# Optimization experiments

Measured on AMD Instinct MI355X. Metric: run time of the kernel, lower is better.

## Reference

```python
import jax, jax.numpy as jnp
import numpy as np

MIN_NORM = 1e-15
BALL_EPS = 4e-3  # float32 boundary eps used by the PoincareBall manifold


def _norm(x):
    return jnp.maximum(jnp.linalg.norm(x, axis=-1, keepdims=True), MIN_NORM)


def _artanh(x):
    # clamp like torch Artanh autograd fn (1e-7 margin)
    return jnp.arctanh(jnp.clip(x, -1.0 + 1e-7, 1.0 - 1e-7))


def proj(x, c):
    n = _norm(x)
    maxnorm = (1.0 - BALL_EPS) / jnp.sqrt(c)
    return jnp.where(n > maxnorm, x / n * maxnorm, x)


def expmap0(u, c):
    sc = jnp.sqrt(c)
    n = _norm(u)
    return jnp.tanh(sc * n) * u / (sc * n)


def logmap0(p, c):
    sc = jnp.sqrt(c)
    n = _norm(p)
    return _artanh(sc * n) * p / (sc * n)


def mobius_add(x, y, c):
    x2 = jnp.sum(x * x, axis=-1, keepdims=True)
    y2 = jnp.sum(y * y, axis=-1, keepdims=True)
    xy = jnp.sum(x * y, axis=-1, keepdims=True)
    num = (1.0 + 2.0 * c * xy + c * y2) * x + (1.0 - c * x2) * y
    denom = 1.0 + 2.0 * c * xy + c * c * x2 * y2
    return num / jnp.maximum(denom, MIN_NORM)


def mobius_matvec(m, x, c):
    sc = jnp.sqrt(c)
    xn = _norm(x)
    mx = x @ m.T  # [N, out]
    mxn = _norm(mx)
    res = jnp.tanh(mxn / xn * _artanh(sc * xn)) * mx / (mxn * sc)
    is_zero = jnp.all(mx == 0, axis=-1, keepdims=True)
    return jnp.where(is_zero, jnp.zeros_like(res), res)


def setup_inputs() -> dict:
    key = jax.random.key(0)
    N, D_IN, D_OUT, E = 100000, 128, 128, 1600000
    k1, k2, k3, k4, k5 = jax.random.split(key, 5)
    # points inside the Poincare ball (||x|| ~ 0.34 < 1)
    x = 0.03 * jax.random.normal(k1, (N, D_IN), dtype=jnp.float32)
    # xavier_uniform with gain sqrt(2)
    limit = np.sqrt(2.0) * np.sqrt(6.0 / (D_IN + D_OUT))
    weight = jax.random.uniform(k2, (D_OUT, D_IN), minval=-limit, maxval=limit, dtype=jnp.float32)
    bias = jnp.zeros((D_OUT,), dtype=jnp.float32)
    edge_index = jax.random.randint(k3, (2, E), 0, N, dtype=jnp.int64)
    edge_weight = jax.random.uniform(k4, (E,), dtype=jnp.float32) / 16.0
    return {"x": x, "weight": weight, "bias": bias,
            "edge_index": edge_index, "edge_weight": edge_weight,
            "num_nodes": N}


def reference(x, weight, bias, edge_index, edge_weight, num_nodes):
    c_in = 1.0
    c_out = 1.0
    # --- OriginHypLinear (dropout=0 / eval) ---
    mv = proj(mobius_matvec(weight, x, c_in), c_in)
    hyp_bias = proj(expmap0(bias[None, :], c_in), c_in)  # proj_tan0 is identity
    h = proj(mobius_add(mv, hyp_bias, c_in), c_in)
    # --- OriginHypAgg: logmap0 -> spmm -> expmap0 ---
    xt = logmap0(h, c_in)
    dst, src = edge_index[0], edge_index[1]
    support = jax.ops.segment_sum(edge_weight[:, None] * xt[src], dst,
                                  num_segments=num_nodes)
    h = proj(expmap0(support, c_in), c_in)
    # --- OriginHypAct: relu in tangent space ---
    xt = jax.nn.relu(logmap0(h, c_in))  # proj_tan0 identity
    return proj(expmap0(xt, c_out), c_out)
```

## Files before the change

### kernel.cpp

```cpp
#include <hip/hip_runtime.h>
#include <math.h>

#define D 128
#define MAXNORM 0.996f
#define MINNORM 1e-15f
#define ATCLAMP (1.0f - 1e-7f)

#define CHUNK 2048
#define BSH   7
#define MAXNB 1024

typedef unsigned int   u32;
typedef unsigned short u16;

typedef __attribute__((ext_vector_type(8))) short bf16x8;
typedef __attribute__((ext_vector_type(4))) float f32x4;

__device__ __forceinline__ float wsum(float v) {
#pragma unroll
  for (int m = 32; m; m >>= 1) v += __shfl_xor(v, m);
  return v;
}
__device__ __forceinline__ float rsum16(float v) {
#pragma unroll
  for (int m = 1; m <= 8; m <<= 1) v += __shfl_xor(v, m);
  return v;
}

__device__ __forceinline__ float frcp(float x) { return __builtin_amdgcn_rcpf(x); }

__device__ __forceinline__ float fast_artanh(float x) {
  x = fminf(x, ATCLAMP);
  return 0.5f * __logf((1.0f + x) * frcp(1.0f - x));
}
__device__ __forceinline__ float fast_tanh(float z) {
  float t = __expf(-2.0f * z);
  return (1.0f - t) * frcp(1.0f + t);
}

__device__ __forceinline__ float bflo(u32 u) { return __uint_as_float(u << 16); }
__device__ __forceinline__ float bfhi(u32 u) { return __uint_as_float(u & 0xffff0000u); }
__device__ __forceinline__ u16 f2bf(float f) {
  u32 u = __float_as_uint(f);
  return (u16)((u + 0x7fffu + ((u >> 16) & 1u)) >> 16);
}
__device__ __forceinline__ float bf2f(u16 h) { return __uint_as_float(((u32)h) << 16); }

union U4B8 { uint4 u; bf16x8 b; };
__device__ __forceinline__ bf16x8 as_b8(uint4 v) { U4B8 c; c.u = v; return c.b; }

__device__ __forceinline__ bool detect_bf16(const u32* p) {
  float lo = fabsf(bflo(p[threadIdx.x & 63]));
  return (bool)__all(lo < 1.0f);
}
__device__ __forceinline__ bool detect_i64(const int* p) {
  return (bool)__all(p[2 * (threadIdx.x & 63) + 1] == 0);
}

template<bool BF>
__device__ __forceinline__ void k1_body(const void* xv, const void* Wv,
                                        const void* bv, u16* xt, int N,
                                        uint4* Wh, uint4* Wl) {
  const int tid  = threadIdx.x;
  const int lane = tid & 63;
  const int wid  = tid >> 6;
  const int qg   = lane >> 4;
  const int lc   = lane & 15;

  for (int slot = tid; slot < 2048; slot += 256) {
    const int l = slot & 63, frag = slot >> 6;
    const int t = frag >> 2, ks = frag & 3;
    const int j  = (l & 15) + 16 * t;
    const int k0 = 32 * ks + 8 * (l >> 4);
    if (BF) {
      Wh[slot] = ((const uint4*)Wv)[j * 16 + (k0 >> 3)];
    } else {
      const float* Wf = (const float*)Wv;
      float4 f0 = *(const float4*)(Wf + (size_t)j * D + k0);
      float4 f1 = *(const float4*)(Wf + (size_t)j * D + k0 + 4);
      float f[8] = {f0.x, f0.y, f0.z, f0.w, f1.x, f1.y, f1.z, f1.w};
      u32 hw[4], lw[4];
#pragma unroll
      for (int i = 0; i < 4; ++i) {
        u16 h0 = f2bf(f[2*i]),  h1 = f2bf(f[2*i+1]);
        u16 l0 = f2bf(f[2*i]   - bf2f(h0));
        u16 l1 = f2bf(f[2*i+1] - bf2f(h1));
        hw[i] = (u32)h0 | ((u32)h1 << 16);
        lw[i] = (u32)l0 | ((u32)l1 << 16);
      }
      Wh[slot] = make_uint4(hw[0], hw[1], hw[2], hw[3]);
      Wl[slot] = make_uint4(lw[0], lw[1], lw[2], lw[3]);
    }
  }

  float bfr[8];
  float nb2 = 0.f;
#pragma unroll
  for (int t = 0; t < 8; ++t) {
    float v = BF ? bf2f(((const u16*)bv)[lc + 16 * t])
                 : ((const float*)bv)[lc + 16 * t];
    bfr[t] = v; nb2 += v * v;
  }
  nb2 = rsum16(nb2);
  float y2;
  {
    float nb = fmaxf(sqrtf(nb2), MINNORM);
    float s  = fast_tanh(nb) * frcp(nb);
    float n1 = s * nb;
    if (n1 > MAXNORM) s *= MAXNORM * frcp(n1);
#pragma unroll
    for (int t = 0; t < 8; ++t) bfr[t] *= s;
    y2 = s * s * nb2;
  }
  const bool bias_zero = (y2 == 0.0f);

  __syncthreads();

  const int tile  = blockIdx.x * 4 + wid;
  const int rbase = tile * 16;
  if (rbase >= N) return;

  int rowA = rbase + lc; if (rowA >= N) rowA = N - 1;
  uint4 Ah[4], Al[4];
  float xn2 = 0.f;
  if (BF) {
    const uint4* xr = (const uint4*)((const u16*)xv + (size_t)rowA * D);
#pragma unroll
    for (int ks = 0; ks < 4; ++ks) {
      uint4 v = xr[4 * ks + qg];
      Ah[ks] = v;
      float a0 = bflo(v.x), a1 = bfhi(v.x), a2 = bflo(v.y), a3 = bfhi(v.y);
      float a4 = bflo(v.z), a5 = bfhi(v.z), a6 = bflo(v.w), a7 = bfhi(v.w);
      xn2 += a0*a0 + a1*a1 + a2*a2 + a3*a3 + a4*a4 + a5*a5 + a6*a6 + a7*a7;
    }
  } else {
    const float4* xr = (const float4*)((const float*)xv + (size_t)rowA * D);
#pragma unroll
    for (int ks = 0; ks < 4; ++ks) {
      float4 f0 = xr[8 * ks + 2 * qg], f1 = xr[8 * ks + 2 * qg + 1];
      float f[8] = {f0.x, f0.y, f0.z, f0.w, f1.x, f1.y, f1.z, f1.w};
      u32 hw[4], lw[4];
#pragma unroll
      for (int i = 0; i < 4; ++i) {
        u16 h0 = f2bf(f[2*i]),  h1 = f2bf(f[2*i+1]);
        u16 l0 = f2bf(f[2*i]   - bf2f(h0));
        u16 l1 = f2bf(f[2*i+1] - bf2f(h1));
        hw[i] = (u32)h0 | ((u32)h1 << 16);
        lw[i] = (u32)l0 | ((u32)l1 << 16);
        xn2 += f[2*i] * f[2*i] + f[2*i+1] * f[2*i+1];
      }
      Ah[ks] = make_uint4(hw[0], hw[1], hw[2], hw[3]);
      Al[ks] = make_uint4(lw[0], lw[1], lw[2], lw[3]);
    }
  }
  xn2 += __shfl_xor(xn2, 16);
  xn2 += __shfl_xor(xn2, 32);

  f32x4 acc[8];
  const f32x4 zero = {0.f, 0.f, 0.f, 0.f};
#pragma unroll
  for (int t = 0; t < 8; ++t) acc[t] = zero;
#pragma unroll
  for (int ks = 0; ks < 4; ++ks) {
    bf16x8 a = as_b8(Ah[ks]);
    bf16x8 al;
    if (!BF) al = as_b8(Al[ks]);
#pragma unroll
    for (int t = 0; t < 8; ++t) {
      const int idx = (t * 4 + ks) * 64 + lane;
      bf16x8 bh = as_b8(Wh[idx]);
      acc[t] = __builtin_amdgcn_mfma_f32_16x16x32_bf16(a, bh, acc[t], 0, 0, 0);
      if (!BF) {
        bf16x8 bl = as_b8(Wl[idx]);
        acc[t] = __builtin_amdgcn_mfma_f32_16x16x32_bf16(al, bh, acc[t], 0, 0, 0);
        acc[t] = __builtin_amdgcn_mfma_f32_16x16x32_bf16(a,  bl, acc[t], 0, 0, 0);
      }
    }
  }

#pragma unroll
  for (int q = 0; q < 4; ++q) {
    const int row_off = qg * 4 + q;
    const int row = rbase + row_off;
    float xnq = fmaxf(sqrtf(__shfl(xn2, row_off)), MINNORM);
    float s2 = 0.f;
#pragma unroll
    for (int t = 0; t < 8; ++t) { float v = acc[t][q]; s2 += v * v; }
    s2 = rsum16(s2);
    float mxn = fmaxf(sqrtf(s2), MINNORM);
    float r = fast_tanh(mxn * frcp(xnq) * fast_artanh(xnq)) * frcp(mxn);
    float pn = r * mxn;
    if (pn > MAXNORM) { r *= MAXNORM * frcp(pn); pn = MAXNORM; }
    float h[8];
    float hn;
    if (bias_zero) {
#pragma unroll
      for (int t = 0; t < 8; ++t) h[t] = r * acc[t][q];
      hn = pn;
    } else {
      float xy = 0.f;
#pragma unroll
      for (int t = 0; t < 8; ++t) { h[t] = r * acc[t][q]; xy += h[t] * bfr[t]; }
      xy = rsum16(xy);
      float x2 = pn * pn;
      float ca = 1.f + 2.f * xy + y2;
      float cb = 1.f - x2;
      float id = frcp(fmaxf(1.f + 2.f * xy + x2 * y2, MINNORM));
      float s3 = 0.f;
#pragma unroll
      for (int t = 0; t < 8; ++t) { h[t] = (ca * h[t] + cb * bfr[t]) * id; s3 += h[t] * h[t]; }
      hn = fmaxf(sqrtf(rsum16(s3)), MINNORM);
    }
    float ps = (hn > MAXNORM) ? (MAXNORM * frcp(hn)) : 1.f;
    float np = fmaxf(hn * ps, MINNORM);
    float tsc = fast_artanh(np) * frcp(np) * ps;
    if (row < N) {
      u16* xo = xt + (size_t)row * D + lc;
#pragma unroll
      for (int t = 0; t < 8; ++t) xo[16 * t] = f2bf(tsc * h[t]);
    }
  }
}

extern "C" __global__ __launch_bounds__(256)
void OriginHyperbolicGraphConvolution_38628935860614_kernel(
    const void* x, const void* W, const void* b, u16* xt, int N) {
  __shared__ uint4 Wh[2048];
  __shared__ uint4 Wl[2048];
  if (detect_bf16((const u32*)x)) k1_body<true >(x, W, b, xt, N, Wh, Wl);
  else                            k1_body<false>(x, W, b, xt, N, Wh, Wl);
}

extern "C" __global__ __launch_bounds__(256) void ks1a(
    const int* ei, u16* cnt, int E, int N, int nb) {
  __shared__ int hist[MAXNB];
  const bool i64 = detect_i64(ei);
  const int tid = threadIdx.x;
  const int cbase = blockIdx.x * CHUNK;
  for (int i = tid; i < MAXNB; i += 256) hist[i] = 0;
  __syncthreads();
#pragma unroll
  for (int r = 0; r < 8; ++r) {
    const int e = cbase + r * 256 + tid;
    if (e < E) {
      int dst, src;
      if (i64) { dst = ei[2 * (size_t)e]; src = ei[2 * ((size_t)E + e)]; }
      else     { dst = ei[e];             src = ei[(size_t)E + e]; }
      if ((unsigned)dst < (unsigned)N && (unsigned)src < (unsigned)N)
        atomicAdd(&hist[dst >> BSH], 1);
    }
  }
  __syncthreads();
  u16* row = cnt + (size_t)blockIdx.x * nb;
  for (int b = tid; b < nb; b += 256) row[b] = (u16)hist[b];
}

extern "C" __global__ __launch_bounds__(256) void ks2sum(
    const u16* cnt, int* btot, int nb, int nchunks) {
  __shared__ int red[256];
  const int b = blockIdx.x, tid = threadIdx.x;
  int s = 0;
  for (int c = tid; c < nchunks; c += 256) s += cnt[(size_t)c * nb + b];
  red[tid] = s; __syncthreads();
#pragma unroll
  for (int off = 128; off; off >>= 1) {
    if (tid < off) red[tid] += red[tid + off];
    __syncthreads();
  }
  if (tid == 0) btot[b] = red[0];
}

extern "C" __global__ __launch_bounds__(1024) void ks2scan(
    const int* btot, int* bbase, int* cursor, int nb) {
  __shared__ int sc[1024];
  const int t = threadIdx.x;
  int v = (t < nb) ? btot[t] : 0;
  sc[t] = v; __syncthreads();
#pragma unroll
  for (int off = 1; off < 1024; off <<= 1) {
    int u = (t >= off) ? sc[t - off] : 0;
    __syncthreads();
    sc[t] += u;
    __syncthreads();
  }
  if (t < nb) { int o = sc[t] - v; bbase[t] = o; cursor[t] = o; }
  if (t == 1023) bbase[nb] = sc[1023];
}

extern "C" __global__ __launch_bounds__(256) void ks1b(
    const int* ei, const void* ew, int* cursor, uint2* ebuck, int E, int N, int nb) {
  __shared__ int   hist[MAXNB];
  __shared__ int   sArr[MAXNB + 1];
  __shared__ int   psum[256];
  __shared__ uint2 recs[CHUNK];
  __shared__ u16   bof[CHUNK];
  const bool i64 = detect_i64(ei);
  const bool bf  = detect_bf16((const u32*)ew);
  const int tid   = threadIdx.x;
  const int cbase = blockIdx.x * CHUNK;

  for (int i = tid; i < MAXNB; i += 256) hist[i] = 0;
  __syncthreads();

  int bkt[8], rank[8]; u32 px[8], wb[8]; bool val[8];
#pragma unroll
  for (int r = 0; r < 8; ++r) {
    const int e = cbase + r * 256 + tid;
    val[r] = false;
    if (e < E) {
      int dst, src;
      if (i64) { dst = ei[2 * (size_t)e]; src = ei[2 * ((size_t)E + e)]; }
      else     { dst = ei[e];             src = ei[(size_t)E + e]; }
      if ((unsigned)dst < (unsigned)N && (unsigned)src < (unsigned)N) {
        val[r] = true;
        bkt[r] = dst >> BSH;
        px[r]  = (u32)src | ((u32)(dst & ((1 << BSH) - 1)) << 17);
        float w;
        if (bf) w = bf2f(((const u16*)ew)[e]); else w = ((const float*)ew)[e];
        wb[r] = __float_as_uint(w);
        rank[r] = atomicAdd(&hist[bkt[r]], 1);
      }
    }
  }
  __syncthreads();

  const int g0 = tid * 4;
  int loc[4], ts = 0;
#pragma unroll
  for (int i = 0; i < 4; ++i) { loc[i] = ts; ts += hist[g0 + i]; }
  psum[tid] = ts; __syncthreads();
#pragma unroll
  for (int off = 1; off < 256; off <<= 1) {
    int t = (tid >= off) ? psum[tid - off] : 0;
    __syncthreads();
    psum[tid] += t;
    __syncthreads();
  }
  const int excl = psum[tid] - ts;
#pragma unroll
  for (int i = 0; i < 4; ++i) sArr[g0 + i] = excl + loc[i];
  if (tid == 255) sArr[MAXNB] = psum[255];
  __syncthreads();

#pragma unroll
  for (int r = 0; r < 8; ++r) if (val[r]) {
    const int idx = sArr[bkt[r]] + rank[r];
    recs[idx] = make_uint2(px[r], wb[r]);
    bof[idx]  = (u16)bkt[r];
  }
  __syncthreads();

  for (int b = tid; b < nb; b += 256) {
    const int c = sArr[b + 1] - sArr[b];
    if (c > 0) hist[b] = atomicAdd(&cursor[b], c);
  }
  const int vcnt = sArr[nb];
  __syncthreads();

  for (int i = tid; i < vcnt; i += 256) {
    const int b = bof[i];
    ebuck[hist[b] + (i - sArr[b])] = recs[i];
  }
}

extern "C" __global__ __launch_bounds__(256) void ks3(
    const uint2* ebuck, const int* bbase, uint2* esrt, int* offs, int N, int nb) {
  __shared__ int hist[128];
  __shared__ int sc[128];
  __shared__ int cur[128];
  const int tid = threadIdx.x;
  const int b = blockIdx.x;
  const int s0 = bbase[b], s1 = bbase[b + 1];
  const int node0 = b << BSH;
  if (tid < 128) hist[tid] = 0;
  __syncthreads();
  for (int i = s0 + tid; i < s1; i += 256)
    atomicAdd(&hist[(ebuck[i].x >> 17) & 127], 1);
  __syncthreads();
  int v = 0;
  if (tid < 128) { v = hist[tid]; sc[tid] = v; }
  __syncthreads();
#pragma unroll
  for (int off = 1; off < 128; off <<= 1) {
    int t = (tid < 128 && tid >= off) ? sc[tid - off] : 0;
    __syncthreads();
    if (tid < 128) sc[tid] += t;
    __syncthreads();
  }
  if (tid < 128) {
    const int st = sc[tid] - v;
    cur[tid] = st;
    const int node = node0 + tid;
    if (node < N) offs[node] = s0 + st;
  }
  if (tid == 0 && b == nb - 1) offs[N] = s1;
  __syncthreads();
  for (int i = s0 + tid; i < s1; i += 256) {
    const uint2 r = ebuck[i];
    const int d = atomicAdd(&cur[(r.x >> 17) & 127], 1);
    esrt[s0 + d] = make_uint2(r.x & 0x1FFFFu, r.y);
  }
}

extern "C" __global__ __launch_bounds__(256) void kagg(
    const int* offs, const uint2* esrt, const u16* xt,
    void* out, const void* xdet, int N) {
  const bool bf = detect_bf16((const u32*)xdet);
  const int lane = threadIdx.x & 63;
  const int node = blockIdx.x * 4 + (threadIdx.x >> 6);
  if (node >= N) return;
  const int s0 = offs[node], s1 = offs[node + 1];
  const u32* xtw = (const u32*)xt;
  float a0 = 0.f, a1 = 0.f;
  for (int base = s0; base < s1; base += 64) {
    const int m = min(64, s1 - base);
    uint2 ed = make_uint2(0u, 0u);
    if (lane < m) ed = esrt[base + lane];
    int i = 0;
    for (; i + 4 <= m; i += 4) {
      const u32 sA = __shfl(ed.x, i),     sB = __shfl(ed.x, i + 1);
      const u32 sC = __shfl(ed.x, i + 2), sD = __shfl(ed.x, i + 3);
      const u32 uA = xtw[(size_t)sA * 64 + lane];
      const u32 uB = xtw[(size_t)sB * 64 + lane];
      const u32 uC = xtw[(size_t)sC * 64 + lane];
      const u32 uD = xtw[(size_t)sD * 64 + lane];
      const float wA = __uint_as_float(__shfl(ed.y, i));
      const float wB = __uint_as_float(__shfl(ed.y, i + 1));
      const float wC = __uint_as_float(__shfl(ed.y, i + 2));
      const float wD = __uint_as_float(__shfl(ed.y, i + 3));
      a0 += wA * bflo(uA) + wB * bflo(uB) + wC * bflo(uC) + wD * bflo(uD);
      a1 += wA * bfhi(uA) + wB * bfhi(uB) + wC * bfhi(uC) + wD * bfhi(uD);
    }
    for (; i < m; ++i) {
      const u32 s = __shfl(ed.x, i);
      const float w = __uint_as_float(__shfl(ed.y, i));
      const u32 u = xtw[(size_t)s * 64 + lane];
      a0 += w * bflo(u);
      a1 += w * bfhi(u);
    }
  }
  float n = fmaxf(sqrtf(wsum(a0 * a0 + a1 * a1)), MINNORM);
  float tn = fast_tanh(n);
  float m = tn * frcp(n);
  if (tn > MAXNORM) { m *= MAXNORM * frcp(tn); tn = MAXNORM; }
  float nn = fmaxf(tn, MINNORM);
  m *= fast_artanh(nn) * frcp(nn);
  float tA = fmaxf(m * a0, 0.f), tB = fmaxf(m * a1, 0.f);
  float nr = fmaxf(sqrtf(wsum(tA * tA + tB * tB)), MINNORM);
  float t2 = fast_tanh(nr);
  float m2 = t2 * frcp(nr);
  if (t2 > MAXNORM) m2 *= MAXNORM * frcp(t2);
  float oA = m2 * tA, oB = m2 * tB;
  if (bf) {
    u32 o = ((u32)f2bf(oA)) | (((u32)f2bf(oB)) << 16);
    ((u32*)out)[(size_t)node * 64 + lane] = o;
  } else {
    ((float2*)out)[(size_t)node * 64 + lane] = make_float2(oA, oB);
  }
}

extern "C" void kernel_launch(void* const* d_in, const int* in_sizes, int n_in,
                              void* d_out, int out_size, void* d_ws, size_t ws_size,
                              hipStream_t stream) {
  const void* x    = d_in[0];
  const void* W    = d_in[1];
  const void* bias = d_in[2];
  const int*  ei   = (const int*)d_in[3];
  const void* ew   = d_in[4];
  const int N = in_sizes[0] / D;
  const int E = in_sizes[4];
  const int nchunks = (E + CHUNK - 1) / CHUNK;
  const int nb      = (N + (1 << BSH) - 1) >> BSH;

  char* ws = (char*)d_ws;
  size_t off = 0;
  auto carve = [&](size_t bytes) { char* p = ws + off; off = (off + bytes + 255) & ~(size_t)255; return p; };
  u16*   xt     = (u16*)  carve((size_t)N * D * sizeof(u16));
  uint2* ebuck  = (uint2*)carve((size_t)E * sizeof(uint2));
  uint2* esrt   = (uint2*)carve((size_t)E * sizeof(uint2));
  u16*   cnt    = (u16*)  carve((size_t)nchunks * nb * sizeof(u16));
  int*   btot   = (int*)  carve((size_t)nb * sizeof(int));
  int*   bbase  = (int*)  carve((size_t)(nb + 1) * sizeof(int));
  int*   cursor = (int*)  carve((size_t)nb * sizeof(int));
  int*   offs   = (int*)  carve((size_t)(N + 1) * sizeof(int));

  OriginHyperbolicGraphConvolution_38628935860614_kernel<<<(N + 63) / 64, 256, 0, stream>>>(
      x, W, bias, xt, N);
  ks1a  <<<nchunks, 256, 0, stream>>>(ei, cnt, E, N, nb);
  ks2sum<<<nb, 256, 0, stream>>>(cnt, btot, nb, nchunks);
  ks2scan<<<1, 1024, 0, stream>>>(btot, bbase, cursor, nb);
  ks1b  <<<nchunks, 256, 0, stream>>>(ei, ew, cursor, ebuck, E, N, nb);
  ks3   <<<nb, 256, 0, stream>>>(ebuck, bbase, esrt, offs, N, nb);
  kagg  <<<(N + 3) / 4, 256, 0, stream>>>(offs, esrt, xt, d_out, x, N);
}
```

Baseline: 280.5 us.

## Replace two-pass bucket sort with chunk-local sort and per-bucket gather

Removes the separate histogram pass (ks1a) that read the edge index a second time. Each chunk now sorts its edges locally by bucket and writes them contiguously along with per-chunk bucket offsets. ks3 gathers each bucket's slices from every chunk into shared memory, with a fallback when a bucket exceeds the staging capacity. kagg now loads edge records directly with wave-uniform offsets and an 8-way unrolled gather instead of shuffles. The cost is many small scattered reads per bucket in ks3, and a 48KB shared staging buffer that lowers occupancy.

```diff
diff --git a/kernel.cpp b/kernel.cpp
--- a/kernel.cpp
+++ b/kernel.cpp
@@ -9,6 +9,7 @@
 #define CHUNK 2048
 #define BSH   7
 #define MAXNB 1024
+#define SCAP  6144
 
 typedef unsigned int   u32;
 typedef unsigned short u16;
@@ -231,69 +232,12 @@
   else                            k1_body<false>(x, W, b, xt, N, Wh, Wl);
 }
 
-extern "C" __global__ __launch_bounds__(256) void ks1a(
-    const int* ei, u16* cnt, int E, int N, int nb) {
-  __shared__ int hist[MAXNB];
-  const bool i64 = detect_i64(ei);
-  const int tid = threadIdx.x;
-  const int cbase = blockIdx.x * CHUNK;
-  for (int i = tid; i < MAXNB; i += 256) hist[i] = 0;
-  __syncthreads();
-#pragma unroll
-  for (int r = 0; r < 8; ++r) {
-    const int e = cbase + r * 256 + tid;
-    if (e < E) {
-      int dst, src;
-      if (i64) { dst = ei[2 * (size_t)e]; src = ei[2 * ((size_t)E + e)]; }
-      else     { dst = ei[e];             src = ei[(size_t)E + e]; }
-      if ((unsigned)dst < (unsigned)N && (unsigned)src < (unsigned)N)
-        atomicAdd(&hist[dst >> BSH], 1);
-    }
-  }
-  __syncthreads();
-  u16* row = cnt + (size_t)blockIdx.x * nb;
-  for (int b = tid; b < nb; b += 256) row[b] = (u16)hist[b];
-}
-
-extern "C" __global__ __launch_bounds__(256) void ks2sum(
-    const u16* cnt, int* btot, int nb, int nchunks) {
-  __shared__ int red[256];
-  const int b = blockIdx.x, tid = threadIdx.x;
-  int s = 0;
-  for (int c = tid; c < nchunks; c += 256) s += cnt[(size_t)c * nb + b];
-  red[tid] = s; __syncthreads();
-#pragma unroll
-  for (int off = 128; off; off >>= 1) {
-    if (tid < off) red[tid] += red[tid + off];
-    __syncthreads();
-  }
-  if (tid == 0) btot[b] = red[0];
-}
-
-extern "C" __global__ __launch_bounds__(1024) void ks2scan(
-    const int* btot, int* bbase, int* cursor, int nb) {
-  __shared__ int sc[1024];
-  const int t = threadIdx.x;
-  int v = (t < nb) ? btot[t] : 0;
-  sc[t] = v; __syncthreads();
-#pragma unroll
-  for (int off = 1; off < 1024; off <<= 1) {
-    int u = (t >= off) ? sc[t - off] : 0;
-    __syncthreads();
-    sc[t] += u;
-    __syncthreads();
-  }
-  if (t < nb) { int o = sc[t] - v; bbase[t] = o; cursor[t] = o; }
-  if (t == 1023) bbase[nb] = sc[1023];
-}
-
-extern "C" __global__ __launch_bounds__(256) void ks1b(
-    const int* ei, const void* ew, int* cursor, uint2* ebuck, int E, int N, int nb) {
+extern "C" __global__ __launch_bounds__(256) void ksA(
+    const int* ei, const void* ew, uint2* ebuck, u16* soffs, int E, int N, int nb) {
   __shared__ int   hist[MAXNB];
   __shared__ int   sArr[MAXNB + 1];
   __shared__ int   psum[256];
   __shared__ uint2 recs[CHUNK];
-  __shared__ u16   bof[CHUNK];
   const bool i64 = detect_i64(ei);
   const bool bf  = detect_bf16((const u32*)ew);
   const int tid   = threadIdx.x;
@@ -343,40 +287,87 @@
   __syncthreads();
 
 #pragma unroll
-  for (int r = 0; r < 8; ++r) if (val[r]) {
-    const int idx = sArr[bkt[r]] + rank[r];
-    recs[idx] = make_uint2(px[r], wb[r]);
-    bof[idx]  = (u16)bkt[r];
-  }
-  __syncthreads();
-
-  for (int b = tid; b < nb; b += 256) {
-    const int c = sArr[b + 1] - sArr[b];
-    if (c > 0) hist[b] = atomicAdd(&cursor[b], c);
-  }
-  const int vcnt = sArr[nb];
-  __syncthreads();
-
-  for (int i = tid; i < vcnt; i += 256) {
-    const int b = bof[i];
-    ebuck[hist[b] + (i - sArr[b])] = recs[i];
-  }
+  for (int r = 0; r < 8; ++r) if (val[r])
+    recs[sArr[bkt[r]] + rank[r]] = make_uint2(px[r], wb[r]);
+  __syncthreads();
+
+  const int vcnt = sArr[MAXNB];
+  for (int i = tid; i < vcnt; i += 256) ebuck[(size_t)cbase + i] = recs[i];
+  u16* so = soffs + (size_t)blockIdx.x * (nb + 1);
+  for (int b = tid; b <= nb; b += 256) so[b] = (u16)sArr[b];
+}
+
+extern "C" __global__ __launch_bounds__(256) void ks2sum(
+    const u16* soffs, int* btot, int nb, int nchunks) {
+  __shared__ int red[256];
+  const int b = blockIdx.x, tid = threadIdx.x;
+  int s = 0;
+  for (int c = tid; c < nchunks; c += 256) {
+    const u16* so = soffs + (size_t)c * (nb + 1) + b;
+    s += (int)so[1] - (int)so[0];
+  }
+  red[tid] = s; __syncthreads();
+#pragma unroll
+  for (int off = 128; off; off >>= 1) {
+    if (tid < off) red[tid] += red[tid + off];
+    __syncthreads();
+  }
+  if (tid == 0) btot[b] = red[0];
+}
+
+extern "C" __global__ __launch_bounds__(1024) void ks2scan(
+    const int* btot, int* bbase, int nb) {
+  __shared__ int sc[1024];
+  const int t = threadIdx.x;
+  int v = (t < nb) ? btot[t] : 0;
+  sc[t] = v; __syncthreads();
+#pragma unroll
+  for (int off = 1; off < 1024; off <<= 1) {
+    int u = (t >= off) ? sc[t - off] : 0;
+    __syncthreads();
+    sc[t] += u;
+    __syncthreads();
+  }
+  if (t < nb) bbase[t] = sc[t] - v;
+  if (t == 1023) bbase[nb] = sc[1023];
 }
 
 extern "C" __global__ __launch_bounds__(256) void ks3(
-    const uint2* ebuck, const int* bbase, uint2* esrt, int* offs, int N, int nb) {
-  __shared__ int hist[128];
-  __shared__ int sc[128];
-  __shared__ int cur[128];
+    const uint2* ebuck, const u16* soffs, const int* bbase,
+    uint2* esrt, int* offs, int N, int nb, int nchunks) {
+  __shared__ uint2 stage[SCAP];
+  __shared__ int hist[128], sc[128], cur[128];
+  __shared__ int lcur;
   const int tid = threadIdx.x;
   const int b = blockIdx.x;
-  const int s0 = bbase[b], s1 = bbase[b + 1];
-  const int node0 = b << BSH;
+  const int s0 = bbase[b], s1 = bbase[b + 1], sz = s1 - s0;
   if (tid < 128) hist[tid] = 0;
-  __syncthreads();
-  for (int i = s0 + tid; i < s1; i += 256)
-    atomicAdd(&hist[(ebuck[i].x >> 17) & 127], 1);
-  __syncthreads();
+  if (tid == 0) lcur = 0;
+  __syncthreads();
+
+  const bool fit = (sz <= SCAP);
+  if (fit) {
+    for (int c = tid; c < nchunks; c += 256) {
+      const u16* so = soffs + (size_t)c * (nb + 1) + b;
+      const int a = so[0], e = so[1];
+      if (e > a) {
+        const int base = atomicAdd(&lcur, e - a);
+        for (int j = a; j < e; ++j) {
+          const uint2 r = ebuck[(size_t)c * CHUNK + j];
+          stage[base + (j - a)] = r;
+          atomicAdd(&hist[(r.x >> 17) & 127], 1);
+        }
+      }
+    }
+  } else {
+    for (int c = tid; c < nchunks; c += 256) {
+      const u16* so = soffs + (size_t)c * (nb + 1) + b;
+      for (int j = so[0]; j < so[1]; ++j)
+        atomicAdd(&hist[(ebuck[(size_t)c * CHUNK + j].x >> 17) & 127], 1);
+    }
+  }
+  __syncthreads();
+
   int v = 0;
   if (tid < 128) { v = hist[tid]; sc[tid] = v; }
   __syncthreads();
@@ -390,15 +381,27 @@
   if (tid < 128) {
     const int st = sc[tid] - v;
     cur[tid] = st;
-    const int node = node0 + tid;
+    const int node = (b << BSH) + tid;
     if (node < N) offs[node] = s0 + st;
   }
   if (tid == 0 && b == nb - 1) offs[N] = s1;
   __syncthreads();
-  for (int i = s0 + tid; i < s1; i += 256) {
-    const uint2 r = ebuck[i];
-    const int d = atomicAdd(&cur[(r.x >> 17) & 127], 1);
-    esrt[s0 + d] = make_uint2(r.x & 0x1FFFFu, r.y);
+
+  if (fit) {
+    for (int i = tid; i < sz; i += 256) {
+      const uint2 r = stage[i];
+      const int d = atomicAdd(&cur[(r.x >> 17) & 127], 1);
+      esrt[s0 + d] = make_uint2(r.x & 0x1FFFFu, r.y);
+    }
+  } else {
+    for (int c = tid; c < nchunks; c += 256) {
+      const u16* so = soffs + (size_t)c * (nb + 1) + b;
+      for (int j = so[0]; j < so[1]; ++j) {
+        const uint2 r = ebuck[(size_t)c * CHUNK + j];
+        const int d = atomicAdd(&cur[(r.x >> 17) & 127], 1);
+        esrt[s0 + d] = make_uint2(r.x & 0x1FFFFu, r.y);
+      }
+    }
   }
 }
 
@@ -409,35 +412,45 @@
   const int lane = threadIdx.x & 63;
   const int node = blockIdx.x * 4 + (threadIdx.x >> 6);
   if (node >= N) return;
-  const int s0 = offs[node], s1 = offs[node + 1];
+  int s0 = __builtin_amdgcn_readfirstlane(offs[node]);
+  int s1 = __builtin_amdgcn_readfirstlane(offs[node + 1]);
+  const uint2* ep = esrt + s0;
+  const int cnt = s1 - s0;
   const u32* xtw = (const u32*)xt;
   float a0 = 0.f, a1 = 0.f;
-  for (int base = s0; base < s1; base += 64) {
-    const int m = min(64, s1 - base);
-    uint2 ed = make_uint2(0u, 0u);
-    if (lane < m) ed = esrt[base + lane];
-    int i = 0;
-    for (; i + 4 <= m; i += 4) {
-      const u32 sA = __shfl(ed.x, i),     sB = __shfl(ed.x, i + 1);
-      const u32 sC = __shfl(ed.x, i + 2), sD = __shfl(ed.x, i + 3);
-      const u32 uA = xtw[(size_t)sA * 64 + lane];
-      const u32 uB = xtw[(size_t)sB * 64 + lane];
-      const u32 uC = xtw[(size_t)sC * 64 + lane];
-      const u32 uD = xtw[(size_t)sD * 64 + lane];
-      const float wA = __uint_as_float(__shfl(ed.y, i));
-      const float wB = __uint_as_float(__shfl(ed.y, i + 1));
-      const float wC = __uint_as_float(__shfl(ed.y, i + 2));
-      const float wD = __uint_as_float(__shfl(ed.y, i + 3));
-      a0 += wA * bflo(uA) + wB * bflo(uB) + wC * bflo(uC) + wD * bflo(uD);
-      a1 += wA * bfhi(uA) + wB * bfhi(uB) + wC * bfhi(uC) + wD * bfhi(uD);
-    }
-    for (; i < m; ++i) {
-      const u32 s = __shfl(ed.x, i);
-      const float w = __uint_as_float(__shfl(ed.y, i));
-      const u32 u = xtw[(size_t)s * 64 + lane];
-      a0 += w * bflo(u);
-      a1 += w * bfhi(u);
-    }
+  int i = 0;
+  for (; i + 8 <= cnt; i += 8) {
+    uint2 e[8]; u32 u[8];
+#pragma unroll
+    for (int k = 0; k < 8; ++k) e[k] = ep[i + k];
+#pragma unroll
+    for (int k = 0; k < 8; ++k) u[k] = xtw[(e[k].x << 6) | lane];
+#pragma unroll
+    for (int k = 0; k < 8; ++k) {
+      const float w = __uint_as_float(e[k].y);
+      a0 += w * bflo(u[k]);
+      a1 += w * bfhi(u[k]);
+    }
+  }
+  for (; i + 4 <= cnt; i += 4) {
+    uint2 e[4]; u32 u[4];
+#pragma unroll
+    for (int k = 0; k < 4; ++k) e[k] = ep[i + k];
+#pragma unroll
+    for (int k = 0; k < 4; ++k) u[k] = xtw[(e[k].x << 6) | lane];
+#pragma unroll
+    for (int k = 0; k < 4; ++k) {
+      const float w = __uint_as_float(e[k].y);
+      a0 += w * bflo(u[k]);
+      a1 += w * bfhi(u[k]);
+    }
+  }
+  for (; i < cnt; ++i) {
+    const uint2 e = ep[i];
+    const u32 u = xtw[(e.x << 6) | lane];
+    const float w = __uint_as_float(e.y);
+    a0 += w * bflo(u);
+    a1 += w * bfhi(u);
   }
   float n = fmaxf(sqrtf(wsum(a0 * a0 + a1 * a1)), MINNORM);
   float tn = fast_tanh(n);
@@ -476,20 +489,18 @@
   size_t off = 0;
   auto carve = [&](size_t bytes) { char* p = ws + off; off = (off + bytes + 255) & ~(size_t)255; return p; };
   u16*   xt     = (u16*)  carve((size_t)N * D * sizeof(u16));
-  uint2* ebuck  = (uint2*)carve((size_t)E * sizeof(uint2));
+  uint2* ebuck  = (uint2*)carve((size_t)nchunks * CHUNK * sizeof(uint2));
   uint2* esrt   = (uint2*)carve((size_t)E * sizeof(uint2));
-  u16*   cnt    = (u16*)  carve((size_t)nchunks * nb * sizeof(u16));
+  u16*   soffs  = (u16*)  carve((size_t)nchunks * (nb + 1) * sizeof(u16));
   int*   btot   = (int*)  carve((size_t)nb * sizeof(int));
   int*   bbase  = (int*)  carve((size_t)(nb + 1) * sizeof(int));
-  int*   cursor = (int*)  carve((size_t)nb * sizeof(int));
   int*   offs   = (int*)  carve((size_t)(N + 1) * sizeof(int));
 
   OriginHyperbolicGraphConvolution_38628935860614_kernel<<<(N + 63) / 64, 256, 0, stream>>>(
       x, W, bias, xt, N);
-  ks1a  <<<nchunks, 256, 0, stream>>>(ei, cnt, E, N, nb);
-  ks2sum<<<nb, 256, 0, stream>>>(cnt, btot, nb, nchunks);
-  ks2scan<<<1, 1024, 0, stream>>>(btot, bbase, cursor, nb);
-  ks1b  <<<nchunks, 256, 0, stream>>>(ei, ew, cursor, ebuck, E, N, nb);
-  ks3   <<<nb, 256, 0, stream>>>(ebuck, bbase, esrt, offs, N, nb);
+  ksA   <<<nchunks, 256, 0, stream>>>(ei, ew, ebuck, soffs, E, N, nb);
+  ks2sum<<<nb, 256, 0, stream>>>(soffs, btot, nb, nchunks);
+  ks2scan<<<1, 1024, 0, stream>>>(btot, bbase, nb);
+  ks3   <<<nb, 256, 0, stream>>>(ebuck, soffs, bbase, esrt, offs, N, nb, nchunks);
   kagg  <<<(N + 3) / 4, 256, 0, stream>>>(offs, esrt, xt, d_out, x, N);
 }
```

New measurement: 271.4 us. -3.3%, faster.
